# Kernel tuning notes

Measured on AMD Instinct MI355X. Metric: run time of the kernel, lower is better.

## Reference

```python
import jax, jax.numpy as jnp
import numpy as np

N = 500000        # total atoms (n1 nodes)
G = 20000         # graphs (g nodes)
D_IN = 128        # in_features
D_H = 256         # hidden width (config_local / mid_features)
D_OUT = 1         # final output per graph (config_global last int)


def setup_inputs() -> dict:
    key = jax.random.key(0)
    ks = jax.random.split(key, 10)
    h = jax.random.normal(ks[0], (N, D_IN), dtype=jnp.float32)
    graph_ids = jnp.sort(jax.random.randint(ks[1], (N,), 0, G))
    s = 0.05
    return {
        "h": h,
        "graph_ids": graph_ids,
        "num_graphs": G,
        # d_local: Linear(128->256) relu, Linear(256->256) relu
        "W1": jax.random.normal(ks[2], (D_IN, D_H), dtype=jnp.float32) * s,
        "b1": jnp.zeros((D_H,), dtype=jnp.float32),
        "W2": jax.random.normal(ks[3], (D_H, D_H), dtype=jnp.float32) * s,
        "b2": jnp.zeros((D_H,), dtype=jnp.float32),
        # d_global: Linear(256->256) relu, Linear(256->1)
        "Wg1": jax.random.normal(ks[4], (D_H, D_H), dtype=jnp.float32) * s,
        "bg1": jnp.zeros((D_H,), dtype=jnp.float32),
        "Wg2": jax.random.normal(ks[5], (D_H, D_OUT), dtype=jnp.float32) * s,
        "bg2": jnp.zeros((D_OUT,), dtype=jnp.float32),
    }


def reference(h, graph_ids, num_graphs, W1, b1, W2, b2, Wg1, bg1, Wg2, bg2):
    # node-level MLP (d_local): h_global per n1 node
    x = jax.nn.relu(h @ W1 + b1)            # [N, D_H]
    x = jax.nn.relu(x @ W2 + b2)            # [N, D_H]
    # copy_src + sum over n1_in_g edges == per-graph segment sum
    pooled = jax.ops.segment_sum(x, graph_ids, num_segments=num_graphs)  # [G, D_H]
    # graph-level MLP (d_global)
    y = jax.nn.relu(pooled @ Wg1 + bg1)     # [G, D_H]
    return y @ Wg2 + bg2                    # [G, 1]
```

## Files before the change

### kernel.cpp

```cpp
#include <hip/hip_runtime.h>
#include <stdint.h>

#define D_IN 128
#define D_H  256
#define BM   64

typedef float f32x4 __attribute__((ext_vector_type(4)));
typedef short s16x8 __attribute__((ext_vector_type(8)));

__device__ __forceinline__ unsigned short f2bf(float x) {
  union { float f; uint32_t u; } v; v.f = x;
  uint32_t r = v.u + 0x7fffu + ((v.u >> 16) & 1u);
  return (unsigned short)(r >> 16);
}

__global__ void prep_kernel(const float* __restrict__ W1, const float* __restrict__ W2,
                            const float* __restrict__ Wg1,
                            float* __restrict__ pooled, unsigned short* __restrict__ W1t,
                            unsigned short* __restrict__ W2t, unsigned short* __restrict__ Wg1t,
                            int pooled_n) {
  int stride = gridDim.x * blockDim.x;
  int tid = blockIdx.x * blockDim.x + threadIdx.x;
  for (int i = tid; i < pooled_n; i += stride) pooled[i] = 0.0f;
  for (int i = tid; i < D_H * D_IN; i += stride) {
    int n = i >> 7, k = i & (D_IN - 1);
    W1t[i] = f2bf(W1[k * D_H + n]);
  }
  for (int i = tid; i < D_H * D_H; i += stride) {
    int n = i >> 8, k = i & (D_H - 1);
    W2t[i]  = f2bf(W2[k * D_H + n]);
    Wg1t[i] = f2bf(Wg1[k * D_H + n]);
  }
}

union NodeSmem {
  struct {
    unsigned short hA[BM][D_IN + 8];
    unsigned short x1[BM][D_H + 8];
  } s;
  float x2[BM][D_H + 4];
};

__global__ __launch_bounds__(256, 2)
void node_kernel(const float* __restrict__ h, const int* __restrict__ gids,
                 const float* __restrict__ b1, const float* __restrict__ b2,
                 const unsigned short* __restrict__ W1t, const unsigned short* __restrict__ W2t,
                 float* __restrict__ pooled, int nnodes) {
  __shared__ NodeSmem sm;
  __shared__ int sgid[BM];
  const int tid  = threadIdx.x;
  const int lane = tid & 63;
  const int wave = tid >> 6;
  const int lr   = lane & 15;
  const int q    = lane >> 4;
  const int row0 = blockIdx.x * BM;

  #pragma unroll
  for (int i = 0; i < 8; ++i) {
    int f4 = tid + i * 256;
    int r  = f4 >> 5;
    int c4 = f4 & 31;
    int gr = row0 + r;
    float4 v = make_float4(0.f, 0.f, 0.f, 0.f);
    if (gr < nnodes) v = ((const float4*)h)[gr * 32 + c4];
    uint32_t p0 = f2bf(v.x) | ((uint32_t)f2bf(v.y) << 16);
    uint32_t p1 = f2bf(v.z) | ((uint32_t)f2bf(v.w) << 16);
    uint32_t* dst = (uint32_t*)&sm.s.hA[r][c4 * 4];
    dst[0] = p0; dst[1] = p1;
  }
  if (tid < BM) {
    int gr = row0 + tid;
    sgid[tid] = (gr < nnodes) ? gids[gr] : -1;
  }
  __syncthreads();

  f32x4 acc[4][4];

  #pragma unroll
  for (int mt = 0; mt < 4; ++mt)
    #pragma unroll
    for (int nt = 0; nt < 4; ++nt)
      acc[mt][nt] = (f32x4){0.f, 0.f, 0.f, 0.f};

  #pragma unroll
  for (int kk = 0; kk < D_IN; kk += 32) {
    const int kq = kk + q * 8;
    s16x8 a[4], b[4];
    #pragma unroll
    for (int mt = 0; mt < 4; ++mt) {
      int f = wave * 64 + mt * 16 + lr;
      a[mt] = *(const s16x8*)&W1t[f * D_IN + kq];
    }
    #pragma unroll
    for (int nt = 0; nt < 4; ++nt)
      b[nt] = *(const s16x8*)&sm.s.hA[nt * 16 + lr][kq];
    #pragma unroll
    for (int mt = 0; mt < 4; ++mt)
      #pragma unroll
      for (int nt = 0; nt < 4; ++nt)
        acc[mt][nt] = __builtin_amdgcn_mfma_f32_16x16x32_bf16(a[mt], b[nt], acc[mt][nt], 0, 0, 0);
  }

  #pragma unroll
  for (int mt = 0; mt < 4; ++mt) {
    int f = wave * 64 + mt * 16 + q * 4;
    float4 bias = *(const float4*)&b1[f];
    #pragma unroll
    for (int nt = 0; nt < 4; ++nt) {
      int nd = nt * 16 + lr;
      float v0 = fmaxf(acc[mt][nt][0] + bias.x, 0.f);
      float v1 = fmaxf(acc[mt][nt][1] + bias.y, 0.f);
      float v2 = fmaxf(acc[mt][nt][2] + bias.z, 0.f);
      float v3 = fmaxf(acc[mt][nt][3] + bias.w, 0.f);
      uint32_t p0 = f2bf(v0) | ((uint32_t)f2bf(v1) << 16);
      uint32_t p1 = f2bf(v2) | ((uint32_t)f2bf(v3) << 16);
      uint32_t* dst = (uint32_t*)&sm.s.x1[nd][f];
      dst[0] = p0; dst[1] = p1;
    }
  }
  __syncthreads();

  #pragma unroll
  for (int mt = 0; mt < 4; ++mt)
    #pragma unroll
    for (int nt = 0; nt < 4; ++nt)
      acc[mt][nt] = (f32x4){0.f, 0.f, 0.f, 0.f};

  #pragma unroll
  for (int kk = 0; kk < D_H; kk += 32) {
    const int kq = kk + q * 8;
    s16x8 a[4], b[4];
    #pragma unroll
    for (int mt = 0; mt < 4; ++mt) {
      int f = wave * 64 + mt * 16 + lr;
      a[mt] = *(const s16x8*)&W2t[f * D_H + kq];
    }
    #pragma unroll
    for (int nt = 0; nt < 4; ++nt)
      b[nt] = *(const s16x8*)&sm.s.x1[nt * 16 + lr][kq];
    #pragma unroll
    for (int mt = 0; mt < 4; ++mt)
      #pragma unroll
      for (int nt = 0; nt < 4; ++nt)
        acc[mt][nt] = __builtin_amdgcn_mfma_f32_16x16x32_bf16(a[mt], b[nt], acc[mt][nt], 0, 0, 0);
  }
  __syncthreads();

  #pragma unroll
  for (int mt = 0; mt < 4; ++mt) {
    int f = wave * 64 + mt * 16 + q * 4;
    float4 bias = *(const float4*)&b2[f];
    #pragma unroll
    for (int nt = 0; nt < 4; ++nt) {
      int nd = nt * 16 + lr;
      f32x4 v;
      v[0] = fmaxf(acc[mt][nt][0] + bias.x, 0.f);
      v[1] = fmaxf(acc[mt][nt][1] + bias.y, 0.f);
      v[2] = fmaxf(acc[mt][nt][2] + bias.z, 0.f);
      v[3] = fmaxf(acc[mt][nt][3] + bias.w, 0.f);
      *(f32x4*)&sm.x2[nd][f] = v;
    }
  }
  __syncthreads();

  float racc = 0.f;
  for (int r = 0; r < BM; ++r) {
    int g = sgid[r];
    if (g >= 0) {
      racc += sm.x2[r][tid];
      if (r == BM - 1 || sgid[r + 1] != g) {
        atomicAdd(&pooled[g * D_H + tid], racc);
        racc = 0.f;
      }
    }
  }
}

union GraphSmem {
  unsigned short pA[BM][D_H + 8];
  float y[BM][D_H + 4];
};

__global__ __launch_bounds__(256, 2)
void graph_kernel(const float* __restrict__ pooled, const float* __restrict__ bg1,
                  const unsigned short* __restrict__ Wg1t, const float* __restrict__ Wg2,
                  const float* __restrict__ bg2, float* __restrict__ out, int ngraphs) {
  __shared__ GraphSmem sm;
  const int tid  = threadIdx.x;
  const int lane = tid & 63;
  const int wave = tid >> 6;
  const int lr   = lane & 15;
  const int q    = lane >> 4;
  const int g0   = blockIdx.x * BM;

  #pragma unroll
  for (int i = 0; i < 16; ++i) {
    int f4 = tid + i * 256;
    int r  = f4 >> 6;
    int c4 = f4 & 63;
    float4 v = make_float4(0.f, 0.f, 0.f, 0.f);
    if (g0 + r < ngraphs) v = ((const float4*)pooled)[(size_t)(g0 + r) * 64 + c4];
    uint32_t p0 = f2bf(v.x) | ((uint32_t)f2bf(v.y) << 16);
    uint32_t p1 = f2bf(v.z) | ((uint32_t)f2bf(v.w) << 16);
    uint32_t* dst = (uint32_t*)&sm.pA[r][c4 * 4];
    dst[0] = p0; dst[1] = p1;
  }
  __syncthreads();

  f32x4 acc[4][4];
  #pragma unroll
  for (int mt = 0; mt < 4; ++mt)
    #pragma unroll
    for (int nt = 0; nt < 4; ++nt)
      acc[mt][nt] = (f32x4){0.f, 0.f, 0.f, 0.f};

  #pragma unroll
  for (int kk = 0; kk < D_H; kk += 32) {
    const int kq = kk + q * 8;
    s16x8 a[4], b[4];
    #pragma unroll
    for (int mt = 0; mt < 4; ++mt) {
      int f = wave * 64 + mt * 16 + lr;
      a[mt] = *(const s16x8*)&Wg1t[f * D_H + kq];
    }
    #pragma unroll
    for (int nt = 0; nt < 4; ++nt)
      b[nt] = *(const s16x8*)&sm.pA[nt * 16 + lr][kq];
    #pragma unroll
    for (int mt = 0; mt < 4; ++mt)
      #pragma unroll
      for (int nt = 0; nt < 4; ++nt)
        acc[mt][nt] = __builtin_amdgcn_mfma_f32_16x16x32_bf16(a[mt], b[nt], acc[mt][nt], 0, 0, 0);
  }
  __syncthreads();

  #pragma unroll
  for (int mt = 0; mt < 4; ++mt) {
    int f = wave * 64 + mt * 16 + q * 4;
    float4 bias = *(const float4*)&bg1[f];
    #pragma unroll
    for (int nt = 0; nt < 4; ++nt) {
      int nd = nt * 16 + lr;
      f32x4 v;
      v[0] = fmaxf(acc[mt][nt][0] + bias.x, 0.f);
      v[1] = fmaxf(acc[mt][nt][1] + bias.y, 0.f);
      v[2] = fmaxf(acc[mt][nt][2] + bias.z, 0.f);
      v[3] = fmaxf(acc[mt][nt][3] + bias.w, 0.f);
      *(f32x4*)&sm.y[nd][f] = v;
    }
  }
  __syncthreads();

  int gloc = tid >> 2;
  int part = tid & 3;
  float p = 0.f;
  #pragma unroll 8
  for (int i = 0; i < 64; ++i) {
    int f = part + 4 * i;
    p += sm.y[gloc][f] * Wg2[f];
  }
  p += __shfl_xor(p, 1);
  p += __shfl_xor(p, 2);
  if (part == 0 && (g0 + gloc) < ngraphs)
    out[g0 + gloc] = p + bg2[0];
}

extern "C" void kernel_launch(void* const* d_in, const int* in_sizes, int n_in,
                              void* d_out, int out_size, void* d_ws, size_t ws_size,
                              hipStream_t stream) {
  const float* h   = (const float*)d_in[0];
  const int*   gid = (const int*)d_in[1];
  const float* W1  = (const float*)d_in[3];
  const float* b1  = (const float*)d_in[4];
  const float* W2  = (const float*)d_in[5];
  const float* b2  = (const float*)d_in[6];
  const float* Wg1 = (const float*)d_in[7];
  const float* bg1 = (const float*)d_in[8];
  const float* Wg2 = (const float*)d_in[9];
  const float* bg2 = (const float*)d_in[10];
  float* out = (float*)d_out;

  const int N = in_sizes[1];
  const int G = out_size;

  char* ws = (char*)d_ws;
  float* pooled = (float*)ws;
  size_t off = (size_t)G * D_H * sizeof(float);
  unsigned short* W1t  = (unsigned short*)(ws + off); off += (size_t)D_H * D_IN * 2;
  unsigned short* W2t  = (unsigned short*)(ws + off); off += (size_t)D_H * D_H * 2;
  unsigned short* Wg1t = (unsigned short*)(ws + off);

  prep_kernel<<<512, 256, 0, stream>>>(W1, W2, Wg1, pooled, W1t, W2t, Wg1t, G * D_H);
  node_kernel<<<(N + BM - 1) / BM, 256, 0, stream>>>(h, gid, b1, b2, W1t, W2t, pooled, N);
  graph_kernel<<<(G + BM - 1) / BM, 256, 0, stream>>>(pooled, bg1, Wg1t, Wg2, bg2, out, G);
}
```

Before: 672.0 us.

## Swizzle node-kernel LDS, preload weight fragments, store second activation in bf16

Replaces the padded shared-memory arrays with XOR-swizzled unpadded bf16 buffers and stores the second-layer activations as bf16 instead of fp32. This shrinks LDS use enough to raise the occupancy hint from 2 to 3 blocks. It also preloads all W1 and W2 weight fragments into registers before each GEMM phase, and reads h with wider nontemporal loads. Keeping the post-ReLU activations in bf16 before pooling adds rounding error to the segment sum, and the larger register arrays may cause spills at the higher occupancy.

```diff
diff --git a/kernel.cpp b/kernel.cpp
--- a/kernel.cpp
+++ b/kernel.cpp
@@ -7,11 +7,17 @@
 
 typedef float f32x4 __attribute__((ext_vector_type(4)));
 typedef short s16x8 __attribute__((ext_vector_type(8)));
+typedef unsigned int u32x2 __attribute__((ext_vector_type(2)));
+typedef unsigned int u32x4 __attribute__((ext_vector_type(4)));
 
 __device__ __forceinline__ unsigned short f2bf(float x) {
   union { float f; uint32_t u; } v; v.f = x;
   uint32_t r = v.u + 0x7fffu + ((v.u >> 16) & 1u);
   return (unsigned short)(r >> 16);
+}
+__device__ __forceinline__ float bf2f(unsigned short u) {
+  union { uint32_t u; float f; } v; v.u = (uint32_t)u << 16;
+  return v.f;
 }
 
 __global__ void prep_kernel(const float* __restrict__ W1, const float* __restrict__ W2,
@@ -33,20 +39,14 @@
   }
 }
 
-union NodeSmem {
-  struct {
-    unsigned short hA[BM][D_IN + 8];
-    unsigned short x1[BM][D_H + 8];
-  } s;
-  float x2[BM][D_H + 4];
-};
-
-__global__ __launch_bounds__(256, 2)
+
+__global__ __launch_bounds__(256, 3)
 void node_kernel(const float* __restrict__ h, const int* __restrict__ gids,
                  const float* __restrict__ b1, const float* __restrict__ b2,
                  const unsigned short* __restrict__ W1t, const unsigned short* __restrict__ W2t,
                  float* __restrict__ pooled, int nnodes) {
-  __shared__ NodeSmem sm;
+  __shared__ unsigned short hA[BM * D_IN];
+  __shared__ unsigned short x1s[BM * D_H];
   __shared__ int sgid[BM];
   const int tid  = threadIdx.x;
   const int lane = tid & 63;
@@ -55,27 +55,40 @@
   const int q    = lane >> 4;
   const int row0 = blockIdx.x * BM;
 
-  #pragma unroll
-  for (int i = 0; i < 8; ++i) {
-    int f4 = tid + i * 256;
-    int r  = f4 >> 5;
-    int c4 = f4 & 31;
-    int gr = row0 + r;
-    float4 v = make_float4(0.f, 0.f, 0.f, 0.f);
-    if (gr < nnodes) v = ((const float4*)h)[gr * 32 + c4];
-    uint32_t p0 = f2bf(v.x) | ((uint32_t)f2bf(v.y) << 16);
-    uint32_t p1 = f2bf(v.z) | ((uint32_t)f2bf(v.w) << 16);
-    uint32_t* dst = (uint32_t*)&sm.s.hA[r][c4 * 4];
-    dst[0] = p0; dst[1] = p1;
-  }
+  s16x8 a[4][4];
+  #pragma unroll
+  for (int ks = 0; ks < 4; ++ks)
+    #pragma unroll
+    for (int mt = 0; mt < 4; ++mt)
+      a[ks][mt] = *(const s16x8*)&W1t[(wave * 64 + mt * 16 + lr) * D_IN + ks * 32 + q * 8];
+
   if (tid < BM) {
     int gr = row0 + tid;
     sgid[tid] = (gr < nnodes) ? gids[gr] : -1;
   }
+
+  #pragma unroll
+  for (int i = 0; i < 4; ++i) {
+    int gi = tid + i * 256;
+    int r  = gi >> 4;
+    int gc = gi & 15;
+    int gr = row0 + r;
+    f32x4 v0 = (f32x4){0.f, 0.f, 0.f, 0.f}, v1 = v0;
+    if (gr < nnodes) {
+      const f32x4* p = (const f32x4*)(h + (size_t)gr * D_IN + gc * 8);
+      v0 = __builtin_nontemporal_load(p);
+      v1 = __builtin_nontemporal_load(p + 1);
+    }
+    u32x4 u;
+    u[0] = f2bf(v0[0]) | ((uint32_t)f2bf(v0[1]) << 16);
+    u[1] = f2bf(v0[2]) | ((uint32_t)f2bf(v0[3]) << 16);
+    u[2] = f2bf(v1[0]) | ((uint32_t)f2bf(v1[1]) << 16);
+    u[3] = f2bf(v1[2]) | ((uint32_t)f2bf(v1[3]) << 16);
+    *(u32x4*)&hA[r * D_IN + ((gc ^ (r & 7)) << 3)] = u;
+  }
   __syncthreads();
 
   f32x4 acc[4][4];
-
   #pragma unroll
   for (int mt = 0; mt < 4; ++mt)
     #pragma unroll
@@ -83,22 +96,17 @@
       acc[mt][nt] = (f32x4){0.f, 0.f, 0.f, 0.f};
 
   #pragma unroll
-  for (int kk = 0; kk < D_IN; kk += 32) {
-    const int kq = kk + q * 8;
-    s16x8 a[4], b[4];
-    #pragma unroll
-    for (int mt = 0; mt < 4; ++mt) {
-      int f = wave * 64 + mt * 16 + lr;
-      a[mt] = *(const s16x8*)&W1t[f * D_IN + kq];
-    }
-    #pragma unroll
-    for (int nt = 0; nt < 4; ++nt)
-      b[nt] = *(const s16x8*)&sm.s.hA[nt * 16 + lr][kq];
+  for (int ks = 0; ks < 4; ++ks) {
+    const int kq = ks * 32 + q * 8;
+    s16x8 b[4];
+    #pragma unroll
+    for (int nt = 0; nt < 4; ++nt)
+      b[nt] = *(const s16x8*)&hA[(nt * 16 + lr) * D_IN + (((kq >> 3) ^ (lr & 7)) << 3)];
     #pragma unroll
     for (int mt = 0; mt < 4; ++mt)
       #pragma unroll
       for (int nt = 0; nt < 4; ++nt)
-        acc[mt][nt] = __builtin_amdgcn_mfma_f32_16x16x32_bf16(a[mt], b[nt], acc[mt][nt], 0, 0, 0);
+        acc[mt][nt] = __builtin_amdgcn_mfma_f32_16x16x32_bf16(a[ks][mt], b[nt], acc[mt][nt], 0, 0, 0);
   }
 
   #pragma unroll
@@ -108,16 +116,20 @@
     #pragma unroll
     for (int nt = 0; nt < 4; ++nt) {
       int nd = nt * 16 + lr;
-      float v0 = fmaxf(acc[mt][nt][0] + bias.x, 0.f);
-      float v1 = fmaxf(acc[mt][nt][1] + bias.y, 0.f);
-      float v2 = fmaxf(acc[mt][nt][2] + bias.z, 0.f);
-      float v3 = fmaxf(acc[mt][nt][3] + bias.w, 0.f);
-      uint32_t p0 = f2bf(v0) | ((uint32_t)f2bf(v1) << 16);
-      uint32_t p1 = f2bf(v2) | ((uint32_t)f2bf(v3) << 16);
-      uint32_t* dst = (uint32_t*)&sm.s.x1[nd][f];
-      dst[0] = p0; dst[1] = p1;
-    }
-  }
+      uint32_t p0 = f2bf(fmaxf(acc[mt][nt][0] + bias.x, 0.f)) |
+                    ((uint32_t)f2bf(fmaxf(acc[mt][nt][1] + bias.y, 0.f)) << 16);
+      uint32_t p1 = f2bf(fmaxf(acc[mt][nt][2] + bias.z, 0.f)) |
+                    ((uint32_t)f2bf(fmaxf(acc[mt][nt][3] + bias.w, 0.f)) << 16);
+      u32x2 w = {p0, p1};
+      *(u32x2*)&x1s[nd * D_H + (((f >> 3) ^ (nd & 7)) << 3) + (f & 7)] = w;
+    }
+  }
+
+  #pragma unroll
+  for (int ks = 0; ks < 4; ++ks)
+    #pragma unroll
+    for (int mt = 0; mt < 4; ++mt)
+      a[ks][mt] = *(const s16x8*)&W2t[(wave * 64 + mt * 16 + lr) * D_H + ks * 32 + q * 8];
   __syncthreads();
 
   #pragma unroll
@@ -127,22 +139,35 @@
       acc[mt][nt] = (f32x4){0.f, 0.f, 0.f, 0.f};
 
   #pragma unroll
-  for (int kk = 0; kk < D_H; kk += 32) {
-    const int kq = kk + q * 8;
-    s16x8 a[4], b[4];
-    #pragma unroll
-    for (int mt = 0; mt < 4; ++mt) {
-      int f = wave * 64 + mt * 16 + lr;
-      a[mt] = *(const s16x8*)&W2t[f * D_H + kq];
-    }
-    #pragma unroll
-    for (int nt = 0; nt < 4; ++nt)
-      b[nt] = *(const s16x8*)&sm.s.x1[nt * 16 + lr][kq];
+  for (int ks = 0; ks < 4; ++ks) {
+    const int kq = ks * 32 + q * 8;
+    s16x8 b[4];
+    #pragma unroll
+    for (int nt = 0; nt < 4; ++nt)
+      b[nt] = *(const s16x8*)&x1s[(nt * 16 + lr) * D_H + (((kq >> 3) ^ (lr & 7)) << 3)];
     #pragma unroll
     for (int mt = 0; mt < 4; ++mt)
       #pragma unroll
       for (int nt = 0; nt < 4; ++nt)
-        acc[mt][nt] = __builtin_amdgcn_mfma_f32_16x16x32_bf16(a[mt], b[nt], acc[mt][nt], 0, 0, 0);
+        acc[mt][nt] = __builtin_amdgcn_mfma_f32_16x16x32_bf16(a[ks][mt], b[nt], acc[mt][nt], 0, 0, 0);
+  }
+  #pragma unroll
+  for (int ks = 0; ks < 4; ++ks)
+    #pragma unroll
+    for (int mt = 0; mt < 4; ++mt)
+      a[ks][mt] = *(const s16x8*)&W2t[(wave * 64 + mt * 16 + lr) * D_H + 128 + ks * 32 + q * 8];
+  #pragma unroll
+  for (int ks = 0; ks < 4; ++ks) {
+    const int kq = 128 + ks * 32 + q * 8;
+    s16x8 b[4];
+    #pragma unroll
+    for (int nt = 0; nt < 4; ++nt)
+      b[nt] = *(const s16x8*)&x1s[(nt * 16 + lr) * D_H + (((kq >> 3) ^ (lr & 7)) << 3)];
+    #pragma unroll
+    for (int mt = 0; mt < 4; ++mt)
+      #pragma unroll
+      for (int nt = 0; nt < 4; ++nt)
+        acc[mt][nt] = __builtin_amdgcn_mfma_f32_16x16x32_bf16(a[ks][mt], b[nt], acc[mt][nt], 0, 0, 0);
   }
   __syncthreads();
 
@@ -153,12 +178,12 @@
     #pragma unroll
     for (int nt = 0; nt < 4; ++nt) {
       int nd = nt * 16 + lr;
-      f32x4 v;
-      v[0] = fmaxf(acc[mt][nt][0] + bias.x, 0.f);
-      v[1] = fmaxf(acc[mt][nt][1] + bias.y, 0.f);
-      v[2] = fmaxf(acc[mt][nt][2] + bias.z, 0.f);
-      v[3] = fmaxf(acc[mt][nt][3] + bias.w, 0.f);
-      *(f32x4*)&sm.x2[nd][f] = v;
+      uint32_t p0 = f2bf(fmaxf(acc[mt][nt][0] + bias.x, 0.f)) |
+                    ((uint32_t)f2bf(fmaxf(acc[mt][nt][1] + bias.y, 0.f)) << 16);
+      uint32_t p1 = f2bf(fmaxf(acc[mt][nt][2] + bias.z, 0.f)) |
+                    ((uint32_t)f2bf(fmaxf(acc[mt][nt][3] + bias.w, 0.f)) << 16);
+      u32x2 w = {p0, p1};
+      *(u32x2*)&x1s[nd * D_H + (((f >> 3) ^ (nd & 7)) << 3) + (f & 7)] = w;
     }
   }
   __syncthreads();
@@ -167,7 +192,7 @@
   for (int r = 0; r < BM; ++r) {
     int g = sgid[r];
     if (g >= 0) {
-      racc += sm.x2[r][tid];
+      racc += bf2f(x1s[r * D_H + (((tid >> 3) ^ (r & 7)) << 3) + (tid & 7)]);
       if (r == BM - 1 || sgid[r + 1] != g) {
         atomicAdd(&pooled[g * D_H + tid], racc);
         racc = 0.f;
```

Result: faster. 579.3 us (-13.8%).
